# Optimization experiments

Measured on AMD Instinct MI355X. Metric: run time of the kernel, lower is better.

## Reference

```python
import jax, jax.numpy as jnp
import numpy as np

N_FEATURES = 512
K = 4
BATCH = 1024

# static upper-triangle pair indices (j1 < j2)
_I1, _I2 = np.triu_indices(N_FEATURES, k=1)
I1 = jnp.asarray(_I1)
I2 = jnp.asarray(_I2)


def setup_inputs() -> dict:
    key = jax.random.key(0)
    kx, kw = jax.random.split(key)
    x = jax.random.normal(kx, (BATCH, N_FEATURES), dtype=jnp.float32)
    # RandomNormal initializer default stddev=0.05
    weight = jax.random.normal(kw, (N_FEATURES, K), dtype=jnp.float32) * 0.05
    return {"x": x, "weight": weight}


def reference(x, weight):
    # per-pair latent dot products: <w_{j1}, w_{j2}> for all j1 < j2  -> [P]
    wdot = jnp.einsum("pk,pk->p", weight[I1], weight[I2])
    # out[b, p] = wdot[p] * x[b, j1(p)] * x[b, j2(p)]  -> [B, P]
    return x[:, I1] * x[:, I2] * wdot[None, :]
```

## Files before the change

kernel.cpp:

```cpp
#include <hip/hip_runtime.h>


#define NF      512
#define KDIM    4
#define BATCH   1024
#define NPAIRS  130816
#define WDPAD   131072
#define TPB     256
#define SPLIT   2
#define PBLK    (WDPAD / SPLIT)
#define NIT     (PBLK / (TPB * 4))
#define BT      16

typedef float f32x4 __attribute__((ext_vector_type(4)));

__device__ __forceinline__ int rowoff(int j) {
    return (j * (1023 - j)) >> 1;
}

__global__ __launch_bounds__(TPB) void fm_wdot(
    const float* __restrict__ w,
    float* __restrict__ wd)
{
    const int j1 = blockIdx.x;
    if (j1 == NF - 1) {
        wd[NPAIRS + threadIdx.x] = 0.f;
        return;
    }
    const int L   = (NF - 1) - j1;
    const int off = rowoff(j1);
    const float wa0 = w[j1*KDIM+0], wa1 = w[j1*KDIM+1],
                wa2 = w[j1*KDIM+2], wa3 = w[j1*KDIM+3];
    for (int t = threadIdx.x; t < L; t += TPB) {
        const int j2 = j1 + 1 + t;
        wd[off + t] = wa0*w[j2*KDIM+0] + wa1*w[j2*KDIM+1]
                    + wa2*w[j2*KDIM+2] + wa3*w[j2*KDIM+3];
    }
}

__global__ __launch_bounds__(TPB) void fm_main2(
    const float* __restrict__ x,
    const float* __restrict__ wd,
    float* __restrict__ out)
{
    __shared__ float xs[NF];

    const int b = blockIdx.x;
    const int t = threadIdx.x;

    if (t < NF / 4)
        reinterpret_cast<f32x4*>(xs)[t] =
            reinterpret_cast<const f32x4*>(x + (size_t)b * NF)[t];
    __syncthreads();

    const int pbase = blockIdx.y * PBLK;
    float* const obase = out + (size_t)b * NPAIRS;

    f32x4 wv = *reinterpret_cast<const f32x4*>(wd + pbase + (t << 2));

    for (int it = 0; it < NIT; ++it) {
        const int p = pbase + it * (TPB * 4) + (t << 2);

        f32x4 nwv = (f32x4){0.f, 0.f, 0.f, 0.f};
        if (it + 1 < NIT)
            nwv = *reinterpret_cast<const f32x4*>(wd + p + TPB * 4);

        if (p < NPAIRS) {
            const float s = sqrtf((float)(1046529 - 8 * p));
            int j1 = (int)((1023.0f - s) * 0.5f);
            j1 = j1 < 0 ? 0 : (j1 > 510 ? 510 : j1);
            int len = 511 - j1;
            int r   = (j1 * (1023 - j1)) >> 1;
            while (r > p)        { --j1; ++len; r -= len; }
            while (p >= r + len) { r += len; --len; ++j1; }

            float xj1 = xs[j1];
            f32x4 o;
            o.x = wv.x * xj1 * xs[p     - r + j1 + 1];
            if (p + 1 >= r + len) { r += len; --len; ++j1; xj1 = xs[j1]; }
            o.y = wv.y * xj1 * xs[p + 1 - r + j1 + 1];
            if (p + 2 >= r + len) { r += len; --len; ++j1; xj1 = xs[j1]; }
            o.z = wv.z * xj1 * xs[p + 2 - r + j1 + 1];
            if (p + 3 >= r + len) { r += len; --len; ++j1; xj1 = xs[j1]; }
            o.w = wv.w * xj1 * xs[p + 3 - r + j1 + 1];

            __builtin_nontemporal_store(o, reinterpret_cast<f32x4*>(obase + p));
        }
        wv = nwv;
    }
}

__global__ __launch_bounds__(TPB) void fm_kernel(
    const float* __restrict__ x,
    const float* __restrict__ w,
    float* __restrict__ out)
{
    const int j1  = blockIdx.x;
    const int b0  = blockIdx.y * BT;
    const int L   = (NF - 1) - j1;
    const int off = j1 * (NF - 1) - (j1 * (j1 - 1)) / 2;

    const float wa0 = w[j1 * KDIM + 0];
    const float wa1 = w[j1 * KDIM + 1];
    const float wa2 = w[j1 * KDIM + 2];
    const float wa3 = w[j1 * KDIM + 3];

    __shared__ float wdl[NF - 1];
    for (int t = threadIdx.x; t < L; t += TPB) {
        const int j2 = j1 + 1 + t;
        wdl[t] = wa0 * w[j2 * KDIM + 0] + wa1 * w[j2 * KDIM + 1]
               + wa2 * w[j2 * KDIM + 2] + wa3 * w[j2 * KDIM + 3];
    }
    __syncthreads();

    for (int bi = 0; bi < BT; ++bi) {
        const int b = b0 + bi;
        const float xj1 = x[(size_t)b * NF + j1];
        const float* __restrict__ xrow = x + (size_t)b * NF + (j1 + 1);
        float* __restrict__ orow = out + (size_t)b * NPAIRS + off;
        for (int t = threadIdx.x; t < L; t += TPB) {
            orow[t] = wdl[t] * xj1 * xrow[t];
        }
    }
}

extern "C" void kernel_launch(void* const* d_in, const int* in_sizes, int n_in,
                              void* d_out, int out_size, void* d_ws, size_t ws_size,
                              hipStream_t stream) {
    const float* x = (const float*)d_in[0];
    const float* w = (const float*)d_in[1];
    float* out = (float*)d_out;

    if (ws_size >= (size_t)WDPAD * sizeof(float)) {
        float* wd = (float*)d_ws;
        fm_wdot<<<dim3(NF), TPB, 0, stream>>>(w, wd);
        fm_main2<<<dim3(BATCH, SPLIT), TPB, 0, stream>>>(x, wd, out);
    } else {
        dim3 grid(NF - 1, BATCH / BT);
        fm_kernel<<<grid, TPB, 0, stream>>>(x, w, out);
    }
}
```

Measured before the change: 532.9 us.

## Precompute packed pair index table and use 2-wide stores in main kernel

Adds a precompute kernel that writes, next to the weight dot products, a packed (j1<<16|j2) index table into the workspace. A new main kernel reads these indices instead of recovering j1 from p with sqrt and correction loops, and writes float2 results with plain stores instead of nontemporal float4 stores. This removes per-element index arithmetic and branching but adds a second table read per output and halves the store width. The old path also drops its nontemporal store. The new path runs only when the workspace holds two tables.

```diff
diff --git a/kernel.cpp b/kernel.cpp
--- a/kernel.cpp
+++ b/kernel.cpp
@@ -9,22 +9,28 @@
 #define TPB     256
 #define SPLIT   2
 #define PBLK    (WDPAD / SPLIT)
-#define NIT     (PBLK / (TPB * 4))
+#define VEC     2
+#define STEP    (TPB * VEC)
+#define NIT     (PBLK / STEP)
 #define BT      16
 
-typedef float f32x4 __attribute__((ext_vector_type(4)));
+typedef float        f32x2 __attribute__((ext_vector_type(2)));
+typedef float        f32x4 __attribute__((ext_vector_type(4)));
+typedef unsigned int u32x2 __attribute__((ext_vector_type(2)));
 
 __device__ __forceinline__ int rowoff(int j) {
     return (j * (1023 - j)) >> 1;
 }
 
-__global__ __launch_bounds__(TPB) void fm_wdot(
+__global__ __launch_bounds__(TPB) void fm_tab(
     const float* __restrict__ w,
-    float* __restrict__ wd)
+    float* __restrict__ wd,
+    unsigned int* __restrict__ idx)
 {
     const int j1 = blockIdx.x;
     if (j1 == NF - 1) {
-        wd[NPAIRS + threadIdx.x] = 0.f;
+        wd[NPAIRS + threadIdx.x]  = 0.f;
+        idx[NPAIRS + threadIdx.x] = 0u;
         return;
     }
     const int L   = (NF - 1) - j1;
@@ -33,14 +39,16 @@
                 wa2 = w[j1*KDIM+2], wa3 = w[j1*KDIM+3];
     for (int t = threadIdx.x; t < L; t += TPB) {
         const int j2 = j1 + 1 + t;
-        wd[off + t] = wa0*w[j2*KDIM+0] + wa1*w[j2*KDIM+1]
-                    + wa2*w[j2*KDIM+2] + wa3*w[j2*KDIM+3];
+        wd[off + t]  = wa0*w[j2*KDIM+0] + wa1*w[j2*KDIM+1]
+                     + wa2*w[j2*KDIM+2] + wa3*w[j2*KDIM+3];
+        idx[off + t] = ((unsigned)j1 << 16) | (unsigned)j2;
     }
 }
 
-__global__ __launch_bounds__(TPB) void fm_main2(
+__global__ __launch_bounds__(TPB) void fm_main3(
     const float* __restrict__ x,
     const float* __restrict__ wd,
+    const unsigned int* __restrict__ idx,
     float* __restrict__ out)
 {
     __shared__ float xs[NF];
@@ -56,15 +64,68 @@
     const int pbase = blockIdx.y * PBLK;
     float* const obase = out + (size_t)b * NPAIRS;
 
+    int p = pbase + (t << 1);
+    f32x2 wv = *reinterpret_cast<const f32x2*>(wd + p);
+    u32x2 iv = *reinterpret_cast<const u32x2*>(idx + p);
+
+    for (int it = 0; it < NIT; ++it, p += STEP) {
+        f32x2 nw = (f32x2){0.f, 0.f};
+        u32x2 ni = (u32x2){0u, 0u};
+        if (it + 1 < NIT) {
+            nw = *reinterpret_cast<const f32x2*>(wd + p + STEP);
+            ni = *reinterpret_cast<const u32x2*>(idx + p + STEP);
+        }
+
+        if (p < NPAIRS) {
+            const int j1a = iv.x >> 16, j2a = iv.x & 0xffff;
+            const int j1b = iv.y >> 16, j2b = iv.y & 0xffff;
+            f32x2 o;
+            o.x = wv.x * xs[j1a] * xs[j2a];
+            o.y = wv.y * xs[j1b] * xs[j2b];
+            *reinterpret_cast<f32x2*>(obase + p) = o;
+        }
+        wv = nw; iv = ni;
+    }
+}
+
+__global__ __launch_bounds__(TPB) void fm_wdot(
+    const float* __restrict__ w, float* __restrict__ wd)
+{
+    const int j1 = blockIdx.x;
+    if (j1 == NF - 1) { wd[NPAIRS + threadIdx.x] = 0.f; return; }
+    const int L   = (NF - 1) - j1;
+    const int off = rowoff(j1);
+    const float wa0 = w[j1*KDIM+0], wa1 = w[j1*KDIM+1],
+                wa2 = w[j1*KDIM+2], wa3 = w[j1*KDIM+3];
+    for (int t = threadIdx.x; t < L; t += TPB) {
+        const int j2 = j1 + 1 + t;
+        wd[off + t] = wa0*w[j2*KDIM+0] + wa1*w[j2*KDIM+1]
+                    + wa2*w[j2*KDIM+2] + wa3*w[j2*KDIM+3];
+    }
+}
+
+__global__ __launch_bounds__(TPB) void fm_main2(
+    const float* __restrict__ x, const float* __restrict__ wd,
+    float* __restrict__ out)
+{
+    __shared__ float xs[NF];
+    const int b = blockIdx.x;
+    const int t = threadIdx.x;
+    if (t < NF / 4)
+        reinterpret_cast<f32x4*>(xs)[t] =
+            reinterpret_cast<const f32x4*>(x + (size_t)b * NF)[t];
+    __syncthreads();
+
+    const int pbase = blockIdx.y * PBLK;
+    float* const obase = out + (size_t)b * NPAIRS;
     f32x4 wv = *reinterpret_cast<const f32x4*>(wd + pbase + (t << 2));
 
-    for (int it = 0; it < NIT; ++it) {
+    const int NIT4 = PBLK / (TPB * 4);
+    for (int it = 0; it < NIT4; ++it) {
         const int p = pbase + it * (TPB * 4) + (t << 2);
-
         f32x4 nwv = (f32x4){0.f, 0.f, 0.f, 0.f};
-        if (it + 1 < NIT)
+        if (it + 1 < NIT4)
             nwv = *reinterpret_cast<const f32x4*>(wd + p + TPB * 4);
-
         if (p < NPAIRS) {
             const float s = sqrtf((float)(1046529 - 8 * p));
             int j1 = (int)((1023.0f - s) * 0.5f);
@@ -73,7 +134,6 @@
             int r   = (j1 * (1023 - j1)) >> 1;
             while (r > p)        { --j1; ++len; r -= len; }
             while (p >= r + len) { r += len; --len; ++j1; }
-
             float xj1 = xs[j1];
             f32x4 o;
             o.x = wv.x * xj1 * xs[p     - r + j1 + 1];
@@ -83,44 +143,36 @@
             o.z = wv.z * xj1 * xs[p + 2 - r + j1 + 1];
             if (p + 3 >= r + len) { r += len; --len; ++j1; xj1 = xs[j1]; }
             o.w = wv.w * xj1 * xs[p + 3 - r + j1 + 1];
-
-            __builtin_nontemporal_store(o, reinterpret_cast<f32x4*>(obase + p));
+            *reinterpret_cast<f32x4*>(obase + p) = o;
         }
         wv = nwv;
     }
 }
 
 __global__ __launch_bounds__(TPB) void fm_kernel(
-    const float* __restrict__ x,
-    const float* __restrict__ w,
+    const float* __restrict__ x, const float* __restrict__ w,
     float* __restrict__ out)
 {
     const int j1  = blockIdx.x;
     const int b0  = blockIdx.y * BT;
     const int L   = (NF - 1) - j1;
     const int off = j1 * (NF - 1) - (j1 * (j1 - 1)) / 2;
-
-    const float wa0 = w[j1 * KDIM + 0];
-    const float wa1 = w[j1 * KDIM + 1];
-    const float wa2 = w[j1 * KDIM + 2];
-    const float wa3 = w[j1 * KDIM + 3];
-
+    const float wa0 = w[j1*KDIM+0], wa1 = w[j1*KDIM+1],
+                wa2 = w[j1*KDIM+2], wa3 = w[j1*KDIM+3];
     __shared__ float wdl[NF - 1];
     for (int t = threadIdx.x; t < L; t += TPB) {
         const int j2 = j1 + 1 + t;
-        wdl[t] = wa0 * w[j2 * KDIM + 0] + wa1 * w[j2 * KDIM + 1]
-               + wa2 * w[j2 * KDIM + 2] + wa3 * w[j2 * KDIM + 3];
+        wdl[t] = wa0*w[j2*KDIM+0] + wa1*w[j2*KDIM+1]
+               + wa2*w[j2*KDIM+2] + wa3*w[j2*KDIM+3];
     }
     __syncthreads();
-
     for (int bi = 0; bi < BT; ++bi) {
         const int b = b0 + bi;
         const float xj1 = x[(size_t)b * NF + j1];
         const float* __restrict__ xrow = x + (size_t)b * NF + (j1 + 1);
         float* __restrict__ orow = out + (size_t)b * NPAIRS + off;
-        for (int t = threadIdx.x; t < L; t += TPB) {
+        for (int t = threadIdx.x; t < L; t += TPB)
             orow[t] = wdl[t] * xj1 * xrow[t];
-        }
     }
 }
 
@@ -131,7 +183,12 @@
     const float* w = (const float*)d_in[1];
     float* out = (float*)d_out;
 
-    if (ws_size >= (size_t)WDPAD * sizeof(float)) {
+    if (ws_size >= 2 * (size_t)WDPAD * sizeof(float)) {
+        float* wd = (float*)d_ws;
+        unsigned int* idx = (unsigned int*)d_ws + WDPAD;
+        fm_tab<<<dim3(NF), TPB, 0, stream>>>(w, wd, idx);
+        fm_main3<<<dim3(BATCH, SPLIT), TPB, 0, stream>>>(x, wd, idx, out);
+    } else if (ws_size >= (size_t)WDPAD * sizeof(float)) {
         float* wd = (float*)d_ws;
         fm_wdot<<<dim3(NF), TPB, 0, stream>>>(w, wd);
         fm_main2<<<dim3(BATCH, SPLIT), TPB, 0, stream>>>(x, wd, out);
```

Result: slower. 576.0 us (+8.1%).

## Flatten output into grid-stride loop over float4 groups, reading x from global

Applied to the files above, without the earlier changes.

Replaces the per-batch-row block layout, which staged x into shared memory and split pairs into two halves, with a persistent grid-stride kernel over the flattened B×P output in float4 groups. Each thread derives batch and pair index with an integer divide, reads wdot and x straight from global/cache, and uses a fast path when all four pairs share the same j1. It also drops the nontemporal store hint in favour of a plain store. The aim is to even out work and improve streaming write bandwidth, at the cost of a per-element divide and uncached global x loads.

```diff
diff --git a/kernel.cpp b/kernel.cpp
--- a/kernel.cpp
+++ b/kernel.cpp
@@ -7,9 +7,9 @@
 #define NPAIRS  130816
 #define WDPAD   131072
 #define TPB     256
-#define SPLIT   2
-#define PBLK    (WDPAD / SPLIT)
-#define NIT     (PBLK / (TPB * 4))
+#define NBLK    2048
+#define NGROUPS 33488896
+#define GSTRIDE (NBLK * TPB)
 #define BT      16
 
 typedef float f32x4 __attribute__((ext_vector_type(4)));
@@ -38,89 +38,79 @@
     }
 }
 
-__global__ __launch_bounds__(TPB) void fm_main2(
+__global__ __launch_bounds__(TPB) void fm_main4(
     const float* __restrict__ x,
     const float* __restrict__ wd,
     float* __restrict__ out)
 {
-    __shared__ float xs[NF];
+    const unsigned t0 = blockIdx.x * TPB + threadIdx.x;
 
-    const int b = blockIdx.x;
-    const int t = threadIdx.x;
+    for (unsigned g = t0; g < NGROUPS; g += GSTRIDE) {
+        const unsigned i = g << 2;
+        const unsigned b = i / NPAIRS;
+        const int p = (int)(i - b * NPAIRS);
 
-    if (t < NF / 4)
-        reinterpret_cast<f32x4*>(xs)[t] =
-            reinterpret_cast<const f32x4*>(x + (size_t)b * NF)[t];
-    __syncthreads();
+        const f32x4 wv = *reinterpret_cast<const f32x4*>(wd + p);
 
-    const int pbase = blockIdx.y * PBLK;
-    float* const obase = out + (size_t)b * NPAIRS;
+        const float s = sqrtf((float)(1046529 - 8 * p));
+        int j1 = (int)((1023.0f - s) * 0.5f);
+        j1 = j1 < 0 ? 0 : (j1 > 510 ? 510 : j1);
+        int len = 511 - j1;
+        int r   = rowoff(j1);
+        while (r > p)        { --j1; ++len; r -= len; }
+        while (p >= r + len) { r += len; --len; ++j1; }
 
-    f32x4 wv = *reinterpret_cast<const f32x4*>(wd + pbase + (t << 2));
-
-    for (int it = 0; it < NIT; ++it) {
-        const int p = pbase + it * (TPB * 4) + (t << 2);
-
-        f32x4 nwv = (f32x4){0.f, 0.f, 0.f, 0.f};
-        if (it + 1 < NIT)
-            nwv = *reinterpret_cast<const f32x4*>(wd + p + TPB * 4);
-
-        if (p < NPAIRS) {
-            const float s = sqrtf((float)(1046529 - 8 * p));
-            int j1 = (int)((1023.0f - s) * 0.5f);
-            j1 = j1 < 0 ? 0 : (j1 > 510 ? 510 : j1);
-            int len = 511 - j1;
-            int r   = (j1 * (1023 - j1)) >> 1;
-            while (r > p)        { --j1; ++len; r -= len; }
-            while (p >= r + len) { r += len; --len; ++j1; }
-
-            float xj1 = xs[j1];
-            f32x4 o;
-            o.x = wv.x * xj1 * xs[p     - r + j1 + 1];
-            if (p + 1 >= r + len) { r += len; --len; ++j1; xj1 = xs[j1]; }
-            o.y = wv.y * xj1 * xs[p + 1 - r + j1 + 1];
-            if (p + 2 >= r + len) { r += len; --len; ++j1; xj1 = xs[j1]; }
-            o.z = wv.z * xj1 * xs[p + 2 - r + j1 + 1];
-            if (p + 3 >= r + len) { r += len; --len; ++j1; xj1 = xs[j1]; }
-            o.w = wv.w * xj1 * xs[p + 3 - r + j1 + 1];
-
-            __builtin_nontemporal_store(o, reinterpret_cast<f32x4*>(obase + p));
+        const float* __restrict__ xrow = x + (size_t)b * NF;
+        const int k = p - r;
+        f32x4 o;
+        if (k + 3 < len) {
+            const float xj1 = xrow[j1];
+            const int j2 = j1 + 1 + k;
+            o.x = wv.x * xj1 * xrow[j2];
+            o.y = wv.y * xj1 * xrow[j2 + 1];
+            o.z = wv.z * xj1 * xrow[j2 + 2];
+            o.w = wv.w * xj1 * xrow[j2 + 3];
+        } else {
+            int rr = r, ll = len, jj = j1;
+            float tmp[4];
+#pragma unroll
+            for (int e = 0; e < 4; ++e) {
+                while (p + e >= rr + ll) { rr += ll; --ll; ++jj; }
+                const int j2 = p + e - rr + jj + 1;
+                const float wde = (e == 0) ? wv.x : (e == 1) ? wv.y
+                                : (e == 2) ? wv.z : wv.w;
+                tmp[e] = wde * xrow[jj] * xrow[j2];
+            }
+            o.x = tmp[0]; o.y = tmp[1]; o.z = tmp[2]; o.w = tmp[3];
         }
-        wv = nwv;
+        *reinterpret_cast<f32x4*>(out + i) = o;
     }
 }
 
 __global__ __launch_bounds__(TPB) void fm_kernel(
-    const float* __restrict__ x,
-    const float* __restrict__ w,
+    const float* __restrict__ x, const float* __restrict__ w,
     float* __restrict__ out)
 {
     const int j1  = blockIdx.x;
     const int b0  = blockIdx.y * BT;
     const int L   = (NF - 1) - j1;
     const int off = j1 * (NF - 1) - (j1 * (j1 - 1)) / 2;
-
-    const float wa0 = w[j1 * KDIM + 0];
-    const float wa1 = w[j1 * KDIM + 1];
-    const float wa2 = w[j1 * KDIM + 2];
-    const float wa3 = w[j1 * KDIM + 3];
-
+    const float wa0 = w[j1*KDIM+0], wa1 = w[j1*KDIM+1],
+                wa2 = w[j1*KDIM+2], wa3 = w[j1*KDIM+3];
     __shared__ float wdl[NF - 1];
     for (int t = threadIdx.x; t < L; t += TPB) {
         const int j2 = j1 + 1 + t;
-        wdl[t] = wa0 * w[j2 * KDIM + 0] + wa1 * w[j2 * KDIM + 1]
-               + wa2 * w[j2 * KDIM + 2] + wa3 * w[j2 * KDIM + 3];
+        wdl[t] = wa0*w[j2*KDIM+0] + wa1*w[j2*KDIM+1]
+               + wa2*w[j2*KDIM+2] + wa3*w[j2*KDIM+3];
     }
     __syncthreads();
-
     for (int bi = 0; bi < BT; ++bi) {
         const int b = b0 + bi;
         const float xj1 = x[(size_t)b * NF + j1];
         const float* __restrict__ xrow = x + (size_t)b * NF + (j1 + 1);
         float* __restrict__ orow = out + (size_t)b * NPAIRS + off;
-        for (int t = threadIdx.x; t < L; t += TPB) {
+        for (int t = threadIdx.x; t < L; t += TPB)
             orow[t] = wdl[t] * xj1 * xrow[t];
-        }
     }
 }
 
@@ -134,7 +124,7 @@
     if (ws_size >= (size_t)WDPAD * sizeof(float)) {
         float* wd = (float*)d_ws;
         fm_wdot<<<dim3(NF), TPB, 0, stream>>>(w, wd);
-        fm_main2<<<dim3(BATCH, SPLIT), TPB, 0, stream>>>(x, wd, out);
+        fm_main4<<<dim3(NBLK), TPB, 0, stream>>>(x, wd, out);
     } else {
         dim3 grid(NF - 1, BATCH / BT);
         fm_kernel<<<grid, TPB, 0, stream>>>(x, w, out);
```

Measured after the change: 576.2 us. +8.1%, slower.
